# Kernel optimization log

Hardware: AMD Instinct MI355X
Metric: run time of the kernel (lower is better)

Reference implementation:

```python
import jax, jax.numpy as jnp
import numpy as np

N_WAY, K_SHOT = 5, 1
N_CLASSES = 64
D = 8


def _conv(x, w, b):
    y = jax.lax.conv_general_dilated(x, w, (2, 2), 'SAME',
                                     dimension_numbers=('NCHW', 'OIHW', 'NCHW'))
    return jax.nn.relu(y + b[None, :, None, None])


def setup_inputs() -> dict:
    key = jax.random.key(0)
    ks = jax.random.split(key, 12)
    b, s_sup, q, h, w = 4, N_WAY * K_SHOT, 1, 64, 64
    rnd = lambda k, shape: jax.random.normal(k, shape, jnp.float32) * 0.05
    return {
        'support_x': jax.random.normal(ks[0], (b, s_sup, 3, h, w), jnp.float32),
        'support_y': jax.random.randint(ks[1], (b, s_sup), 0, N_CLASSES),
        'query_x': jax.random.normal(ks[2], (b, q, 3, h, w), jnp.float32),
        'query_y': jax.random.randint(ks[3], (b, q), 0, N_CLASSES),
        'k1': rnd(ks[4], (32, 3, 3, 3)), 'bc1': jnp.zeros((32,), jnp.float32),
        'k2': rnd(ks[5], (48, 32, 3, 3)), 'bc2': jnp.zeros((48,), jnp.float32),
        'k3': rnd(ks[6], (64, 48, 3, 3)), 'bc3': jnp.zeros((64,), jnp.float32),
        'Wlog': rnd(ks[7], (64, N_CLASSES)), 'blog': jnp.zeros((N_CLASSES,), jnp.float32),
        'Wg1': rnd(ks[8], (132, 128)), 'bg1': jnp.zeros((128,), jnp.float32),
        'Wg2': rnd(ks[9], (128, 64)), 'bg2': jnp.zeros((64,), jnp.float32),
        'Wf1': rnd(ks[10], (64, 16)), 'bf1': jnp.zeros((16,), jnp.float32),
        'Wf2': rnd(ks[11], (16, 1)), 'bf2': jnp.zeros((1,), jnp.float32),
    }


def reference(support_x, support_y, query_x, query_y,
              k1, bc1, k2, bc2, k3, bc3, Wlog, blog,
              Wg1, bg1, Wg2, bg2, Wf1, bf1, Wf2, bf2):
    x = jnp.concatenate([support_x, query_x], axis=1)       # [b, s, 3, h, w]
    label = jnp.concatenate([support_y, query_y], axis=1)   # [b, s]
    b, s = label.shape
    h, w = x.shape[-2:]

    feat = x.reshape(b * s, 3, h, w)
    feat = _conv(feat, k1, bc1)
    feat = _conv(feat, k2, bc2)
    feat = _conv(feat, k3, bc3)                              # [b*s, c, D, D]
    c = feat.shape[1]
    logits = feat.mean(axis=(2, 3)) @ Wlog + blog            # [b*s, n_classes]

    # --- append normalized (i/d, j/d) coord channels ---
    ii = jnp.arange(D, dtype=feat.dtype) / D
    coord = jnp.stack([jnp.broadcast_to(ii[:, None], (D, D)),
                       jnp.broadcast_to(ii[None, :], (D, D))])        # [2, D, D]
    feat = feat.reshape(b, s, c, D, D)
    feat = jnp.concatenate([feat, jnp.broadcast_to(coord, (b, s, 2, D, D))], axis=2)
    c2 = c + 2
    m = D * D
    a = feat.reshape(b, s, c2, m).transpose(0, 1, 3, 2)      # [b, s, m, c2]

    # --- relation network g over all (set-pair, position-pair) combos ---
    # original: g(concat(x_i, x_j)) where x_i = x[b, j, :, q], x_j = x[b, i, :, p]
    # split first linear: concat @ Wg1 = x_i @ Wg1[:c2] + x_j @ Wg1[c2:]
    W1a, W1b = Wg1[:c2], Wg1[c2:]
    u = a @ W1a                                              # [b, s_j, m_q, 128]
    v = a @ W1b + bg1                                        # [b, s_i, m_p, 128]
    # hdd[b,i,j,q,p] = relu(u[b,j,q] + v[b,i,p])  -> [b, s, s, m, m, 128]
    hdd = jax.nn.relu(u[:, None, :, :, None, :] + v[:, :, None, None, :, :])
    g = jax.nn.relu(hdd @ Wg2 + bg2)                         # [b, s, s, m, m, 64]
    x_f = g.sum(axis=(3, 4))                                 # [b, s, s, 64]
    score = jax.nn.sigmoid(jax.nn.relu(x_f @ Wf1 + bf1) @ Wf2 + bf2)  # [b, s, s, 1]

    # --- losses ---
    logp = jax.nn.log_softmax(logits, axis=-1)
    lab = label.reshape(-1)
    cls_loss = -jnp.take_along_axis(logp, lab[:, None], axis=1).mean()

    y = (label[:, :, None] == label[:, None, :])[..., None].astype(score.dtype)
    P = score[..., 0]                                        # [b, s, s]
    Pt = P.transpose(0, 2, 1)
    sym, anti = 0.5 * (P + Pt), 0.5 * (P - Pt)
    sym_n = jnp.sqrt((sym ** 2).sum(axis=(1, 2)))            # Frobenius per batch
    anti_n = jnp.sqrt((anti ** 2).sum(axis=(1, 2)))
    sym_loss = ((sym_n - anti_n) / (sym_n + anti_n)).mean()
    euc_loss = ((score - y) ** 2).mean()
    rn_loss = euc_loss - 0.1 * sym_loss
    return (cls_loss, rn_loss, sym_loss)
```

## Files before the change

### kernel.cpp

```cpp
#include <hip/hip_runtime.h>

typedef _Float16 f16x8 __attribute__((ext_vector_type(8)));
typedef float f32x4 __attribute__((ext_vector_type(4)));
typedef unsigned u32x4 __attribute__((ext_vector_type(4)));

#define NB 192

__device__ __forceinline__ float ldw(const float* p) {
    return __uint_as_float(__hip_atomic_load((unsigned*)p, __ATOMIC_RELAXED,
                                             __HIP_MEMORY_SCOPE_SYSTEM));
}
__device__ __forceinline__ void stw(float* p, float x) {
    __hip_atomic_store((unsigned*)p, __float_as_uint(x), __ATOMIC_RELAXED,
                       __HIP_MEMORY_SCOPE_SYSTEM);
}
__device__ __forceinline__ unsigned ldu(const unsigned* p) {
    return __hip_atomic_load((unsigned*)p, __ATOMIC_RELAXED, __HIP_MEMORY_SCOPE_SYSTEM);
}
__device__ __forceinline__ void stu(unsigned* p, unsigned x) {
    __hip_atomic_store(p, x, __ATOMIC_RELAXED, __HIP_MEMORY_SCOPE_SYSTEM);
}

__device__ __forceinline__ void postf(int* fl, int bid) {
    asm volatile("s_waitcnt vmcnt(0) lgkmcnt(0)" ::: "memory");
    __hip_atomic_store(fl + bid, 1, __ATOMIC_RELAXED, __HIP_MEMORY_SCOPE_SYSTEM);
}
__device__ __forceinline__ void gbar(int* fl, int bid, int tid) {
    __syncthreads();
    if (tid == 0) postf(fl, bid);
    if (tid < 64) {
        int* p0 = fl + tid;
        for (;;) {
            int ok = (__hip_atomic_load(p0, __ATOMIC_RELAXED, __HIP_MEMORY_SCOPE_SYSTEM) == 1)
                   & (__hip_atomic_load(p0+64, __ATOMIC_RELAXED, __HIP_MEMORY_SCOPE_SYSTEM) == 1)
                   & (__hip_atomic_load(p0+128, __ATOMIC_RELAXED, __HIP_MEMORY_SCOPE_SYSTEM) == 1);
            if (__all(ok)) break;
            __builtin_amdgcn_s_sleep(2);
        }
    }
    __syncthreads();
    asm volatile("" ::: "memory");
}

__global__ void __launch_bounds__(512) mega3_k(
    const float* __restrict__ sx, const int* __restrict__ sy,
    const float* __restrict__ qx, const int* __restrict__ qy,
    const float* __restrict__ k1, const float* __restrict__ bc1,
    const float* __restrict__ k2, const float* __restrict__ bc2,
    const float* __restrict__ k3, const float* __restrict__ bc3,
    const float* __restrict__ Wlog, const float* __restrict__ blog,
    const float* __restrict__ Wg1, const float* __restrict__ bg1,
    const float* __restrict__ Wg2, const float* __restrict__ bg2,
    const float* __restrict__ Wf1, const float* __restrict__ bf1,
    const float* __restrict__ Wf2, const float* __restrict__ bf2,
    float* __restrict__ ws, float* __restrict__ out)
{
    __shared__ __align__(16) float smem[32768];
    const int tid = threadIdx.x;
    const int bid = blockIdx.x;

    float* feat1 = ws;
    float* feat2 = feat1 + 786432;
    float* feat3 = feat2 + 294912;
    float* mf    = feat3 + 98304;
    float* rv    = mf + 1536;
    float* Pmg   = rv + 64;
    unsigned* U32 = (unsigned*)(Pmg + 160);
    unsigned* V32 = U32 + 98304;
    int* flag0 = (int*)(V32 + 98304);
    int* flag1 = flag0 + 192;
    int* flag2 = flag1 + 192;
    int* flag3 = flag2 + 192;
    int* flagB = flag3 + 192;

    {
        int n = bid >> 3, ocq = bid & 7;
        int bi = n / 6, si = n % 6;
        const float* inp = (si < 5) ? sx + (size_t)((bi*5+si)*3)*4096
                                    : qx + (size_t)(bi*3)*4096;
        #pragma unroll
        for (int half = 0; half < 2; half++) {
            int px = tid + half*512;
            int oy = px >> 5, ox = px & 31;
            float tap[27];
            #pragma unroll
            for (int ic = 0; ic < 3; ic++)
                #pragma unroll
                for (int dy = 0; dy < 3; dy++)
                    #pragma unroll
                    for (int dx = 0; dx < 3; dx++) {
                        int iy = 2*oy+dy, ix = 2*ox+dx;
                        tap[ic*9+dy*3+dx] = (iy < 64 && ix < 64) ? inp[ic*4096 + iy*64 + ix] : 0.f;
                    }
            #pragma unroll
            for (int l = 0; l < 4; l++) {
                int oc = ocq*4 + l;
                float acc = bc1[oc];
                #pragma unroll
                for (int t = 0; t < 27; t++) acc += tap[t]*k1[oc*27 + t];
                stw(&feat1[(size_t)(n*32+oc)*1024 + px], fmaxf(acc, 0.f));
            }
        }
    }
    gbar(flag0, bid, tid);

    if (bid < 144) {
        int img = bid / 6, ocg = bid % 6;
        for (int k = 0; k < 64; k++) {
            int e = tid + 512*k;
            smem[e] = ldw(&feat1[(size_t)img*32768 + e]);
        }
        __syncthreads();
        int osub = tid >> 8, px = tid & 255;
        int oy = px >> 4, ox = px & 15;
        int ocb = ocg*8 + osub*4;
        float a0 = bc2[ocb], a1 = bc2[ocb+1], a2 = bc2[ocb+2], a3 = bc2[ocb+3];
        for (int ic = 0; ic < 32; ic++) {
            float tap[9];
            #pragma unroll
            for (int dy = 0; dy < 3; dy++)
                #pragma unroll
                for (int dx = 0; dx < 3; dx++) {
                    int iy = 2*oy+dy, ix = 2*ox+dx;
                    tap[dy*3+dx] = (iy < 32 && ix < 32) ? smem[ic*1024 + iy*32 + ix] : 0.f;
                }
            const float* wb = k2 + (size_t)ocb*288 + ic*9;
            #pragma unroll
            for (int t = 0; t < 9; t++) {
                a0 += tap[t]*wb[t];
                a1 += tap[t]*wb[288+t];
                a2 += tap[t]*wb[576+t];
                a3 += tap[t]*wb[864+t];
            }
        }
        size_t ob = (size_t)(img*48 + ocb)*256 + px;
        stw(&feat2[ob      ], fmaxf(a0, 0.f));
        stw(&feat2[ob + 256], fmaxf(a1, 0.f));
        stw(&feat2[ob + 512], fmaxf(a2, 0.f));
        stw(&feat2[ob + 768], fmaxf(a3, 0.f));
    }
    gbar(flag1, bid, tid);

    {
        int img = bid >> 3, ocg = bid & 7;
        __syncthreads();
        for (int k = 0; k < 24; k++) {
            int e = tid + 512*k;
            smem[e] = ldw(&feat2[(size_t)img*12288 + e]);
        }
        __syncthreads();
        int osub = tid >> 6, px = tid & 63;
        int oy = px >> 3, ox = px & 7;
        int oc = ocg*8 + osub;
        float a0 = bc3[oc];
        for (int ic = 0; ic < 48; ic++) {
            const float* wb = k3 + (size_t)oc*432 + ic*9;
            #pragma unroll
            for (int dy = 0; dy < 3; dy++)
                #pragma unroll
                for (int dx = 0; dx < 3; dx++) {
                    int iy = 2*oy+dy, ix = 2*ox+dx;
                    float tv = (iy < 16 && ix < 16) ? smem[ic*256 + iy*16 + ix] : 0.f;
                    a0 += tv * wb[dy*3+dx];
                }
        }
        float r0 = fmaxf(a0, 0.f);
        stw(&feat3[(size_t)(img*64 + oc)*64 + px], r0);
        #pragma unroll
        for (int off = 32; off >= 1; off >>= 1) r0 += __shfl_xor(r0, off, 64);
        if (px == 0) stw(&mf[img*64 + oc], r0 * (1.f/64.f));
    }
    gbar(flag2, bid, tid);

    if (bid < 48) {
        int bs = bid >> 1, ph = bid & 1;
        for (int k = 0; k < 8; k++) {
            int e = tid + 512*k;
            smem[e] = ldw(&feat3[(size_t)bs*4096 + e]);
        }
        __syncthreads();
        int cp = tid & 63;
        int sel = (tid >> 6) & 1;
        int pq = tid >> 7;
        int pbase = ph*32 + pq*8;
        float acc0[8], acc1[8];
        float b0 = sel ? bg1[2*cp] : 0.f;
        float b1 = sel ? bg1[2*cp+1] : 0.f;
        #pragma unroll
        for (int k = 0; k < 8; k++) { acc0[k] = b0; acc1[k] = b1; }
        const float* Wc = Wg1 + sel*66*128 + 2*cp;
        for (int c = 0; c < 64; c++) {
            float w0 = Wc[c*128], w1 = Wc[c*128 + 1];
            #pragma unroll
            for (int k = 0; k < 8; k++) {
                float a = smem[c*64 + pbase + k];
                acc0[k] += a*w0; acc1[k] += a*w1;
            }
        }
        #pragma unroll
        for (int c = 64; c < 66; c++) {
            float w0 = Wc[c*128], w1 = Wc[c*128 + 1];
            #pragma unroll
            for (int k = 0; k < 8; k++) {
                int p = pbase + k;
                float a = (c == 64) ? (float)(p>>3)*0.125f : (float)(p&7)*0.125f;
                acc0[k] += a*w0; acc1[k] += a*w1;
            }
        }
        unsigned* dst = sel ? V32 : U32;
        #pragma unroll
        for (int k = 0; k < 8; k++) {
            int p = pbase + k;
            unsigned lo = (unsigned)__builtin_bit_cast(unsigned short, (_Float16)acc0[k]);
            unsigned hi = (unsigned)__builtin_bit_cast(unsigned short, (_Float16)acc1[k]);
            stu(&dst[(size_t)bs*4096 + p*64 + cp], lo | (hi << 16));
        }
    } else if (bid < 72 && tid < 64) {
        int n = bid - 48;
        float s = blog[tid];
        for (int c = 0; c < 64; c++) s += ldw(&mf[n*64 + c]) * Wlog[c*64 + tid];
        float mx = s;
        #pragma unroll
        for (int off = 32; off >= 1; off >>= 1) mx = fmaxf(mx, __shfl_xor(mx, off, 64));
        float p = __expf(s - mx);
        float se = p;
        #pragma unroll
        for (int off = 32; off >= 1; off >>= 1) se += __shfl_xor(se, off, 64);
        int bi = n/6, si = n%6;
        int lab = (si < 5) ? sy[bi*5+si] : qy[bi];
        float s_lab = __shfl(s, lab, 64);
        if (tid == 0) stw(&rv[n], -(s_lab - mx - __logf(se)));
    }
    if (bid >= 144) {
        __syncthreads();
        if (tid == 0) postf(flag3, bid);
        return;
    }
    gbar(flag3, bid, tid);

    {
        int cb = bid;
        int b = cb / 36, rem = cb % 36;
        int j = rem / 6, i = rem % 6;
        int lane = tid & 63, wv8 = tid >> 6;
        int col = lane & 15, quad = lane >> 4;
        int qhalf = wv8 >> 2, pw = wv8 & 3;

        _Float16* Vsh = (_Float16*)smem;
        unsigned* Vsh32 = (unsigned*)smem;
        float* xfred = smem + 4096;
        float* xfl   = smem + 4608;
        float* hidl  = smem + 4672;

        int uimg = b*6 + i, vimg = b*6 + j;
        __syncthreads();
        #pragma unroll
        for (int k = 0; k < 8; k++) {
            int e = tid + 512*k;
            Vsh32[e] = ldu(&V32[(size_t)vimg*4096 + e]);
        }
        f16x8 uf[4];
        {
            const unsigned* up = U32 + (size_t)uimg*4096 + (pw*16 + col)*64 + quad*4;
            #pragma unroll
            for (int kt = 0; kt < 4; kt++) {
                u32x4 t;
                #pragma unroll
                for (int r = 0; r < 4; r++) t[r] = ldu(&up[kt*16 + r]);
                uf[kt] = __builtin_bit_cast(f16x8, t);
            }
        }
        f16x8 bf[4][4];
        #pragma unroll
        for (int kt = 0; kt < 4; kt++)
            #pragma unroll
            for (int nt = 0; nt < 4; nt++) {
                f16x8 t;
                #pragma unroll
                for (int jj = 0; jj < 8; jj++)
                    t[jj] = (_Float16)Wg2[(kt*32 + quad*8 + jj)*64 + nt*16 + col];
                bf[kt][nt] = t;
            }
        float bgv[4];
        #pragma unroll
        for (int nt = 0; nt < 4; nt++) bgv[nt] = bg2[nt*16 + col];
        __syncthreads();

        float sums[4] = {0.f,0.f,0.f,0.f};
        for (int qq = 0; qq < 32; qq++) {
            int q = qhalf*32 + qq;
            const _Float16* vp = &Vsh[q*128 + quad*8];
            f32x4 acc[4];
            #pragma unroll
            for (int nt = 0; nt < 4; nt++)
                acc[nt] = (f32x4){bgv[nt], bgv[nt], bgv[nt], bgv[nt]};
            #pragma unroll
            for (int kt = 0; kt < 4; kt++) {
                f16x8 vf = *(const f16x8*)&vp[kt*32];
                f16x8 af = uf[kt] + vf;
                af = __builtin_elementwise_max(af, (f16x8){0,0,0,0,0,0,0,0});
                #pragma unroll
                for (int nt = 0; nt < 4; nt++)
                    acc[nt] = __builtin_amdgcn_mfma_f32_16x16x32_f16(af, bf[kt][nt], acc[nt], 0, 0, 0);
            }
            #pragma unroll
            for (int nt = 0; nt < 4; nt++)
                #pragma unroll
                for (int rr = 0; rr < 4; rr++)
                    sums[nt] += fmaxf(acc[nt][rr], 0.f);
        }
        #pragma unroll
        for (int nt = 0; nt < 4; nt++) {
            sums[nt] += __shfl_xor(sums[nt], 16, 64);
            sums[nt] += __shfl_xor(sums[nt], 32, 64);
        }
        if (lane < 16) {
            #pragma unroll
            for (int nt = 0; nt < 4; nt++) xfred[wv8*64 + nt*16 + lane] = sums[nt];
        }
        __syncthreads();
        if (tid < 64) {
            float x = 0.f;
            #pragma unroll
            for (int w8 = 0; w8 < 8; w8++) x += xfred[w8*64 + tid];
            xfl[tid] = x;
        }
        __syncthreads();
        if (tid < 16) {
            float s = bf1[tid];
            for (int c = 0; c < 64; c++) s += xfl[c]*Wf1[c*16 + tid];
            hidl[tid] = fmaxf(s, 0.f);
        }
        __syncthreads();
        if (tid == 0) {
            float sc = bf2[0];
            #pragma unroll
            for (int h = 0; h < 16; h++) sc += hidl[h]*Wf2[h];
            stw(&Pmg[cb], 1.f/(1.f + __expf(-sc)));
            postf(flagB, cb);
        }
    }

    if (bid == 0) {
        if (tid < 64) {
            int* p0 = flagB + tid;
            for (;;) {
                int ok = (__hip_atomic_load(p0, __ATOMIC_RELAXED, __HIP_MEMORY_SCOPE_SYSTEM) == 1)
                       & (__hip_atomic_load(p0+64, __ATOMIC_RELAXED, __HIP_MEMORY_SCOPE_SYSTEM) == 1)
                       & ((tid < 16) ? (__hip_atomic_load(p0+128, __ATOMIC_RELAXED, __HIP_MEMORY_SCOPE_SYSTEM) == 1) : 1);
                if (__all(ok)) break;
                __builtin_amdgcn_s_sleep(2);
            }
        }
        __syncthreads();
        asm volatile("" ::: "memory");

        float* Pmsh = smem;
        int*   lab  = (int*)(smem + 160);
        float* red  = smem + 192;
        float* ratio= smem + 768;
        if (tid < 144) Pmsh[tid] = ldw(&Pmg[tid]);
        if (tid < 24) { int bi = tid/6, si = tid%6; lab[tid] = (si < 5) ? sy[bi*5+si] : qy[bi]; }
        __syncthreads();
        float e = 0.f;
        if (tid < 144) {
            int b = tid/36, r = tid%36, jj = r/6, ii = r%6;
            float y = (lab[b*6+jj] == lab[b*6+ii]) ? 1.f : 0.f;
            float d = Pmsh[tid] - y;
            e = d*d;
        }
        red[tid] = e;
        __syncthreads();
        for (int s = 256; s > 0; s >>= 1) {
            if (tid < s) red[tid] += red[tid+s];
            __syncthreads();
        }
        if (tid < 4) {
            float s2 = 0.f, a2 = 0.f;
            for (int jj = 0; jj < 6; jj++)
                for (int ii = 0; ii < 6; ii++) {
                    float pa = Pmsh[tid*36 + jj*6 + ii], pb = Pmsh[tid*36 + ii*6 + jj];
                    float sm = 0.5f*(pa+pb), an = 0.5f*(pa-pb);
                    s2 += sm*sm; a2 += an*an;
                }
            float sn = sqrtf(s2), anq = sqrtf(a2);
            ratio[tid] = (sn - anq)/(sn + anq);
        }
        __syncthreads();
        if (tid == 0) {
            float sl = 0.25f*(ratio[0]+ratio[1]+ratio[2]+ratio[3]);
            float euc = red[0] * (1.f/144.f);
            float cs = 0.f;
            for (int k = 0; k < 24; k++) cs += ldw(&rv[k]);
            out[0] = cs * (1.f/24.f);
            out[1] = euc - 0.1f*sl;
            out[2] = sl;
        }
    }
}

extern "C" void kernel_launch(void* const* d_in, const int* in_sizes, int n_in,
                              void* d_out, int out_size, void* d_ws, size_t ws_size,
                              hipStream_t stream) {
    (void)in_sizes; (void)n_in; (void)out_size; (void)ws_size;
    const float* sx   = (const float*)d_in[0];
    const int*   sy   = (const int*)  d_in[1];
    const float* qx   = (const float*)d_in[2];
    const int*   qy   = (const int*)  d_in[3];
    const float* k1   = (const float*)d_in[4];
    const float* bc1  = (const float*)d_in[5];
    const float* k2   = (const float*)d_in[6];
    const float* bc2  = (const float*)d_in[7];
    const float* k3   = (const float*)d_in[8];
    const float* bc3  = (const float*)d_in[9];
    const float* Wlog = (const float*)d_in[10];
    const float* blog = (const float*)d_in[11];
    const float* Wg1  = (const float*)d_in[12];
    const float* bg1  = (const float*)d_in[13];
    const float* Wg2  = (const float*)d_in[14];
    const float* bg2  = (const float*)d_in[15];
    const float* Wf1  = (const float*)d_in[16];
    const float* bf1  = (const float*)d_in[17];
    const float* Wf2  = (const float*)d_in[18];
    const float* bf2  = (const float*)d_in[19];
    float* ws  = (float*)d_ws;
    float* out = (float*)d_out;

    mega3_k<<<NB, 512, 0, stream>>>(sx, sy, qx, qy, k1, bc1, k2, bc2,
                                    k3, bc3, Wlog, blog, Wg1, bg1, Wg2, bg2,
                                    Wf1, bf1, Wf2, bf2, ws, out);
}
```

Baseline: 196.6 us.

## Restructure conv2/conv3 stages with row-register reuse, swizzled LDS, and 64-bit loads

Conv2 and conv3 are remapped so that each thread computes a whole output row for one output channel over a slice of input channels. Each thread loads input rows from LDS as float4 vectors into registers and reuses them across the 3 horizontal taps. Partial sums from the channel slices are then reduced through LDS. The LDS tile uses an XOR swizzle to reduce bank conflicts on the vector reads. All cross-block workspace loads switch from 32-bit to 64-bit relaxed atomic loads, which halves the number of load instructions. The cost is more registers, extra LDS reduction passes and syncs, and more complex indexing.

Measured after the change: 425.0 us. 116% more time.

```diff
diff --git a/kernel.cpp b/kernel.cpp
--- a/kernel.cpp
+++ b/kernel.cpp
@@ -2,7 +2,7 @@
 
 typedef _Float16 f16x8 __attribute__((ext_vector_type(8)));
 typedef float f32x4 __attribute__((ext_vector_type(4)));
-typedef unsigned u32x4 __attribute__((ext_vector_type(4)));
+typedef unsigned long long u64;
 
 #define NB 192
 
@@ -14,13 +14,9 @@
     __hip_atomic_store((unsigned*)p, __float_as_uint(x), __ATOMIC_RELAXED,
                        __HIP_MEMORY_SCOPE_SYSTEM);
 }
-__device__ __forceinline__ unsigned ldu(const unsigned* p) {
-    return __hip_atomic_load((unsigned*)p, __ATOMIC_RELAXED, __HIP_MEMORY_SCOPE_SYSTEM);
-}
-__device__ __forceinline__ void stu(unsigned* p, unsigned x) {
-    __hip_atomic_store(p, x, __ATOMIC_RELAXED, __HIP_MEMORY_SCOPE_SYSTEM);
-}
-
+__device__ __forceinline__ u64 ld64(const u64* p) {
+    return __hip_atomic_load(p, __ATOMIC_RELAXED, __HIP_MEMORY_SCOPE_SYSTEM);
+}
 __device__ __forceinline__ void postf(int* fl, int bid) {
     asm volatile("s_waitcnt vmcnt(0) lgkmcnt(0)" ::: "memory");
     __hip_atomic_store(fl + bid, 1, __ATOMIC_RELAXED, __HIP_MEMORY_SCOPE_SYSTEM);
@@ -42,7 +38,7 @@
     asm volatile("" ::: "memory");
 }
 
-__global__ void __launch_bounds__(512) mega3_k(
+__global__ void __launch_bounds__(512) mega4_k(
     const float* __restrict__ sx, const int* __restrict__ sy,
     const float* __restrict__ qx, const int* __restrict__ qy,
     const float* __restrict__ k1, const float* __restrict__ bc1,
@@ -106,77 +102,146 @@
 
     if (bid < 144) {
         int img = bid / 6, ocg = bid % 6;
-        for (int k = 0; k < 64; k++) {
-            int e = tid + 512*k;
-            smem[e] = ldw(&feat1[(size_t)img*32768 + e]);
-        }
-        __syncthreads();
-        int osub = tid >> 8, px = tid & 255;
-        int oy = px >> 4, ox = px & 15;
-        int ocb = ocg*8 + osub*4;
-        float a0 = bc2[ocb], a1 = bc2[ocb+1], a2 = bc2[ocb+2], a3 = bc2[ocb+3];
-        for (int ic = 0; ic < 32; ic++) {
-            float tap[9];
-            #pragma unroll
-            for (int dy = 0; dy < 3; dy++)
-                #pragma unroll
-                for (int dx = 0; dx < 3; dx++) {
-                    int iy = 2*oy+dy, ix = 2*ox+dx;
-                    tap[dy*3+dx] = (iy < 32 && ix < 32) ? smem[ic*1024 + iy*32 + ix] : 0.f;
+        const u64* src = (const u64*)(feat1 + (size_t)img*32768);
+        for (int b = 0; b < 4; b++) {
+            u64 t[8];
+            #pragma unroll
+            for (int j = 0; j < 8; j++) t[j] = ld64(&src[b*4096 + j*512 + tid]);
+            #pragma unroll
+            for (int j = 0; j < 8; j++) {
+                int d = (b*4096 + j*512 + tid)*2;
+                int ic = d >> 10, r = d & 1023, iy = r >> 5, ix = r & 31;
+                int la = (ic<<10) + (iy<<5) + (((((ix>>2)) ^ ((iy>>1)&7))<<2) | (ix&3));
+                ((u64*)smem)[la>>1] = t[j];
+            }
+        }
+        __syncthreads();
+        int oy = tid & 15, ocl = (tid>>4) & 7, ich = tid >> 7;
+        int oc = ocg*8 + ocl;
+        float acc[16];
+        #pragma unroll
+        for (int x = 0; x < 16; x++) acc[x] = 0.f;
+        for (int ic = ich*8; ic < ich*8+8; ic++) {
+            #pragma unroll
+            for (int dy = 0; dy < 3; dy++) {
+                int iy = 2*oy + dy;
+                float row[33];
+                if (iy < 32) {
+                    int sw = (iy>>1) & 7;
+                    #pragma unroll
+                    for (int q = 0; q < 8; q++) {
+                        f32x4 v = *(const f32x4*)&smem[(ic<<10) + (iy<<5) + ((q^sw)<<2)];
+                        row[q*4] = v[0]; row[q*4+1] = v[1]; row[q*4+2] = v[2]; row[q*4+3] = v[3];
+                    }
+                    row[32] = 0.f;
+                } else {
+                    #pragma unroll
+                    for (int x = 0; x < 33; x++) row[x] = 0.f;
                 }
-            const float* wb = k2 + (size_t)ocb*288 + ic*9;
-            #pragma unroll
-            for (int t = 0; t < 9; t++) {
-                a0 += tap[t]*wb[t];
-                a1 += tap[t]*wb[288+t];
-                a2 += tap[t]*wb[576+t];
-                a3 += tap[t]*wb[864+t];
-            }
-        }
-        size_t ob = (size_t)(img*48 + ocb)*256 + px;
-        stw(&feat2[ob      ], fmaxf(a0, 0.f));
-        stw(&feat2[ob + 256], fmaxf(a1, 0.f));
-        stw(&feat2[ob + 512], fmaxf(a2, 0.f));
-        stw(&feat2[ob + 768], fmaxf(a3, 0.f));
+                const float* wp = k2 + (size_t)oc*288 + ic*9 + dy*3;
+                float w0 = wp[0], w1 = wp[1], w2 = wp[2];
+                #pragma unroll
+                for (int ox = 0; ox < 16; ox++)
+                    acc[ox] += row[2*ox]*w0 + row[2*ox+1]*w1 + row[2*ox+2]*w2;
+            }
+        }
+        __syncthreads();
+        #pragma unroll
+        for (int q = 0; q < 4; q++)
+            *(f32x4*)&smem[ich*2048 + ocl*256 + oy*16 + q*4] =
+                (f32x4){acc[q*4], acc[q*4+1], acc[q*4+2], acc[q*4+3]};
+        __syncthreads();
+        #pragma unroll
+        for (int r = 0; r < 4; r++) {
+            int o = r*512 + tid;
+            float s = smem[o] + smem[2048+o] + smem[4096+o] + smem[6144+o];
+            int ocl2 = o >> 8, px = o & 255;
+            s += bc2[ocg*8 + ocl2];
+            stw(&feat2[(size_t)(img*48 + ocg*8 + ocl2)*256 + px], fmaxf(s, 0.f));
+        }
     }
     gbar(flag1, bid, tid);
 
     {
         int img = bid >> 3, ocg = bid & 7;
         __syncthreads();
-        for (int k = 0; k < 24; k++) {
-            int e = tid + 512*k;
-            smem[e] = ldw(&feat2[(size_t)img*12288 + e]);
-        }
-        __syncthreads();
-        int osub = tid >> 6, px = tid & 63;
-        int oy = px >> 3, ox = px & 7;
-        int oc = ocg*8 + osub;
-        float a0 = bc3[oc];
-        for (int ic = 0; ic < 48; ic++) {
-            const float* wb = k3 + (size_t)oc*432 + ic*9;
-            #pragma unroll
-            for (int dy = 0; dy < 3; dy++)
-                #pragma unroll
-                for (int dx = 0; dx < 3; dx++) {
-                    int iy = 2*oy+dy, ix = 2*ox+dx;
-                    float tv = (iy < 16 && ix < 16) ? smem[ic*256 + iy*16 + ix] : 0.f;
-                    a0 += tv * wb[dy*3+dx];
+        const u64* src = (const u64*)(feat2 + (size_t)img*12288);
+        for (int b = 0; b < 2; b++) {
+            u64 t[8];
+            #pragma unroll
+            for (int j = 0; j < 8; j++) {
+                int idx = b*4096 + j*512 + tid;
+                if (idx < 6144) t[j] = ld64(&src[idx]);
+            }
+            #pragma unroll
+            for (int j = 0; j < 8; j++) {
+                int idx = b*4096 + j*512 + tid;
+                if (idx < 6144) {
+                    int d = idx*2;
+                    int ic = d >> 8, r = d & 255, iy = r >> 4, ix = r & 15;
+                    int la = (ic<<8) + (iy<<4) + (((((ix>>2)) ^ ((iy>>1)&3))<<2) | (ix&3));
+                    ((u64*)smem)[la>>1] = t[j];
                 }
-        }
-        float r0 = fmaxf(a0, 0.f);
-        stw(&feat3[(size_t)(img*64 + oc)*64 + px], r0);
-        #pragma unroll
-        for (int off = 32; off >= 1; off >>= 1) r0 += __shfl_xor(r0, off, 64);
-        if (px == 0) stw(&mf[img*64 + oc], r0 * (1.f/64.f));
+            }
+        }
+        __syncthreads();
+        int oy = tid & 7, ocl = (tid>>3) & 7, ich = tid >> 6;
+        int oc = ocg*8 + ocl;
+        float acc[8];
+        #pragma unroll
+        for (int x = 0; x < 8; x++) acc[x] = 0.f;
+        for (int ic = ich*6; ic < ich*6+6; ic++) {
+            #pragma unroll
+            for (int dy = 0; dy < 3; dy++) {
+                int iy = 2*oy + dy;
+                float row[17];
+                if (iy < 16) {
+                    int sw = (iy>>1) & 3;
+                    #pragma unroll
+                    for (int q = 0; q < 4; q++) {
+                        f32x4 v = *(const f32x4*)&smem[(ic<<8) + (iy<<4) + ((q^sw)<<2)];
+                        row[q*4] = v[0]; row[q*4+1] = v[1]; row[q*4+2] = v[2]; row[q*4+3] = v[3];
+                    }
+                    row[16] = 0.f;
+                } else {
+                    #pragma unroll
+                    for (int x = 0; x < 17; x++) row[x] = 0.f;
+                }
+                const float* wp = k3 + (size_t)oc*432 + ic*9 + dy*3;
+                float w0 = wp[0], w1 = wp[1], w2 = wp[2];
+                #pragma unroll
+                for (int ox = 0; ox < 8; ox++)
+                    acc[ox] += row[2*ox]*w0 + row[2*ox+1]*w1 + row[2*ox+2]*w2;
+            }
+        }
+        __syncthreads();
+        *(f32x4*)&smem[ich*512 + ocl*64 + oy*8]     = (f32x4){acc[0],acc[1],acc[2],acc[3]};
+        *(f32x4*)&smem[ich*512 + ocl*64 + oy*8 + 4] = (f32x4){acc[4],acc[5],acc[6],acc[7]};
+        __syncthreads();
+        {
+            int ocl2 = tid >> 6, px = tid & 63;
+            float s = bc3[ocg*8 + ocl2];
+            #pragma unroll
+            for (int h = 0; h < 8; h++) s += smem[h*512 + tid];
+            float r0 = fmaxf(s, 0.f);
+            stw(&feat3[(size_t)(img*64 + ocg*8 + ocl2)*64 + px], r0);
+            #pragma unroll
+            for (int off = 32; off >= 1; off >>= 1) r0 += __shfl_xor(r0, off, 64);
+            if (px == 0) stw(&mf[img*64 + ocg*8 + ocl2], r0 * (1.f/64.f));
+        }
     }
     gbar(flag2, bid, tid);
 
     if (bid < 48) {
         int bs = bid >> 1, ph = bid & 1;
-        for (int k = 0; k < 8; k++) {
-            int e = tid + 512*k;
-            smem[e] = ldw(&feat3[(size_t)bs*4096 + e]);
+        __syncthreads();
+        const u64* src = (const u64*)(feat3 + (size_t)bs*4096);
+        {
+            u64 t[4];
+            #pragma unroll
+            for (int j = 0; j < 4; j++) t[j] = ld64(&src[j*512 + tid]);
+            #pragma unroll
+            for (int j = 0; j < 4; j++) ((u64*)smem)[j*512 + tid] = t[j];
         }
         __syncthreads();
         int cp = tid & 63;
@@ -213,7 +278,8 @@
             int p = pbase + k;
             unsigned lo = (unsigned)__builtin_bit_cast(unsigned short, (_Float16)acc0[k]);
             unsigned hi = (unsigned)__builtin_bit_cast(unsigned short, (_Float16)acc1[k]);
-            stu(&dst[(size_t)bs*4096 + p*64 + cp], lo | (hi << 16));
+            __hip_atomic_store(&dst[(size_t)bs*4096 + p*64 + cp], lo | (hi << 16),
+                               __ATOMIC_RELAXED, __HIP_MEMORY_SCOPE_SYSTEM);
         }
     } else if (bid < 72 && tid < 64) {
         int n = bid - 48;
@@ -247,27 +313,33 @@
         int qhalf = wv8 >> 2, pw = wv8 & 3;
 
         _Float16* Vsh = (_Float16*)smem;
-        unsigned* Vsh32 = (unsigned*)smem;
         float* xfred = smem + 4096;
         float* xfl   = smem + 4608;
         float* hidl  = smem + 4672;
 
         int uimg = b*6 + i, vimg = b*6 + j;
         __syncthreads();
-        #pragma unroll
-        for (int k = 0; k < 8; k++) {
-            int e = tid + 512*k;
-            Vsh32[e] = ldu(&V32[(size_t)vimg*4096 + e]);
+        {
+            const u64* src = (const u64*)(V32 + (size_t)vimg*4096);
+            u64 t[4];
+            #pragma unroll
+            for (int k = 0; k < 4; k++) t[k] = ld64(&src[k*512 + tid]);
+            #pragma unroll
+            for (int k = 0; k < 4; k++) ((u64*)smem)[k*512 + tid] = t[k];
         }
         f16x8 uf[4];
         {
-            const unsigned* up = U32 + (size_t)uimg*4096 + (pw*16 + col)*64 + quad*4;
+            const u64* up = (const u64*)(U32 + (size_t)uimg*4096 + (pw*16 + col)*64 + quad*4);
+            u64 t[8];
             #pragma unroll
             for (int kt = 0; kt < 4; kt++) {
-                u32x4 t;
-                #pragma unroll
-                for (int r = 0; r < 4; r++) t[r] = ldu(&up[kt*16 + r]);
-                uf[kt] = __builtin_bit_cast(f16x8, t);
+                t[kt*2]   = ld64(&up[kt*8]);
+                t[kt*2+1] = ld64(&up[kt*8 + 1]);
+            }
+            #pragma unroll
+            for (int kt = 0; kt < 4; kt++) {
+                u64 pair[2] = {t[kt*2], t[kt*2+1]};
+                uf[kt] = __builtin_bit_cast(f16x8, pair);
             }
         }
         f16x8 bf[4][4];
@@ -426,7 +498,7 @@
     float* ws  = (float*)d_ws;
     float* out = (float*)d_out;
 
-    mega3_k<<<NB, 512, 0, stream>>>(sx, sy, qx, qy, k1, bc1, k2, bc2,
+    mega4_k<<<NB, 512, 0, stream>>>(sx, sy, qx, qy, k1, bc1, k2, bc2,
                                     k3, bc3, Wlog, blog, Wg1, bg1, Wg2, bg2,
                                     Wf1, bf1, Wf2, bf2, ws, out);
 }
```

## Fuse per-image backbone and projection into one block with per-image dataflow flags

Applied to the files above, without the earlier changes.

Each of 24 images now runs conv1, conv2, conv3, the Wg1 projection and the classification logits entirely in one block's shared memory, instead of spreading each stage over 192 blocks joined by grid-wide barriers and global feature buffers. Pair blocks then wait only on flags for the two images they need rather than on a full grid barrier, and the grid shrinks to 144 blocks. This removes global round trips for intermediate features and most barrier latency, at the cost of much less parallelism in the backbone (24 blocks doing all the conv work) and a serial chain per image.

Result: slower. 288.0 us (+46.5%).

```diff
diff --git a/kernel.cpp b/kernel.cpp
--- a/kernel.cpp
+++ b/kernel.cpp
@@ -4,8 +4,6 @@
 typedef float f32x4 __attribute__((ext_vector_type(4)));
 typedef unsigned u32x4 __attribute__((ext_vector_type(4)));
 
-#define NB 192
-
 __device__ __forceinline__ float ldw(const float* p) {
     return __uint_as_float(__hip_atomic_load((unsigned*)p, __ATOMIC_RELAXED,
                                              __HIP_MEMORY_SCOPE_SYSTEM));
@@ -20,29 +18,15 @@
 __device__ __forceinline__ void stu(unsigned* p, unsigned x) {
     __hip_atomic_store(p, x, __ATOMIC_RELAXED, __HIP_MEMORY_SCOPE_SYSTEM);
 }
-
-__device__ __forceinline__ void postf(int* fl, int bid) {
+__device__ __forceinline__ void postf(int* fl, int idx) {
     asm volatile("s_waitcnt vmcnt(0) lgkmcnt(0)" ::: "memory");
-    __hip_atomic_store(fl + bid, 1, __ATOMIC_RELAXED, __HIP_MEMORY_SCOPE_SYSTEM);
-}
-__device__ __forceinline__ void gbar(int* fl, int bid, int tid) {
-    __syncthreads();
-    if (tid == 0) postf(fl, bid);
-    if (tid < 64) {
-        int* p0 = fl + tid;
-        for (;;) {
-            int ok = (__hip_atomic_load(p0, __ATOMIC_RELAXED, __HIP_MEMORY_SCOPE_SYSTEM) == 1)
-                   & (__hip_atomic_load(p0+64, __ATOMIC_RELAXED, __HIP_MEMORY_SCOPE_SYSTEM) == 1)
-                   & (__hip_atomic_load(p0+128, __ATOMIC_RELAXED, __HIP_MEMORY_SCOPE_SYSTEM) == 1);
-            if (__all(ok)) break;
-            __builtin_amdgcn_s_sleep(2);
-        }
-    }
-    __syncthreads();
-    asm volatile("" ::: "memory");
-}
-
-__global__ void __launch_bounds__(512) mega3_k(
+    __hip_atomic_store(fl + idx, 1, __ATOMIC_RELAXED, __HIP_MEMORY_SCOPE_SYSTEM);
+}
+__device__ __forceinline__ int ldflag(const int* fl, int idx) {
+    return __hip_atomic_load(fl + idx, __ATOMIC_RELAXED, __HIP_MEMORY_SCOPE_SYSTEM);
+}
+
+__global__ void __launch_bounds__(512) mega5_k(
     const float* __restrict__ sx, const int* __restrict__ sy,
     const float* __restrict__ qx, const int* __restrict__ qy,
     const float* __restrict__ k1, const float* __restrict__ bc1,
@@ -59,23 +43,16 @@
     const int tid = threadIdx.x;
     const int bid = blockIdx.x;
 
-    float* feat1 = ws;
-    float* feat2 = feat1 + 786432;
-    float* feat3 = feat2 + 294912;
-    float* mf    = feat3 + 98304;
-    float* rv    = mf + 1536;
+    float* rv    = ws;
     float* Pmg   = rv + 64;
     unsigned* U32 = (unsigned*)(Pmg + 160);
-    unsigned* V32 = U32 + 98304;
-    int* flag0 = (int*)(V32 + 98304);
-    int* flag1 = flag0 + 192;
-    int* flag2 = flag1 + 192;
-    int* flag3 = flag2 + 192;
-    int* flagB = flag3 + 192;
-
-    {
-        int n = bid >> 3, ocq = bid & 7;
-        int bi = n / 6, si = n % 6;
+    unsigned* V32 = U32 + 24*4096;
+    int* flagC   = (int*)(V32 + 24*4096);
+    int* flagB   = flagC + 64;
+
+    if (bid < 24) {
+        const int n = bid;
+        const int bi = n / 6, si = n % 6;
         const float* inp = (si < 5) ? sx + (size_t)((bi*5+si)*3)*4096
                                     : qx + (size_t)(bi*3)*4096;
         #pragma unroll
@@ -92,156 +69,146 @@
                         int iy = 2*oy+dy, ix = 2*ox+dx;
                         tap[ic*9+dy*3+dx] = (iy < 64 && ix < 64) ? inp[ic*4096 + iy*64 + ix] : 0.f;
                     }
-            #pragma unroll
-            for (int l = 0; l < 4; l++) {
-                int oc = ocq*4 + l;
-                float acc = bc1[oc];
-                #pragma unroll
-                for (int t = 0; t < 27; t++) acc += tap[t]*k1[oc*27 + t];
-                stw(&feat1[(size_t)(n*32+oc)*1024 + px], fmaxf(acc, 0.f));
-            }
-        }
+            for (int oc = 0; oc < 32; oc++) {
+                float a = bc1[oc];
+                #pragma unroll
+                for (int t = 0; t < 27; t++) a += tap[t]*k1[oc*27 + t];
+                smem[oc*1024 + px] = fmaxf(a, 0.f);
+            }
+        }
+        __syncthreads();
+
+        {
+            int px = tid & 255, grp = tid >> 8;
+            int oy = px >> 4, ox = px & 15;
+            float acc[24];
+            #pragma unroll
+            for (int o = 0; o < 24; o++) acc[o] = bc2[grp*24 + o];
+            for (int ic = 0; ic < 32; ic++) {
+                float tap[9];
+                #pragma unroll
+                for (int dy = 0; dy < 3; dy++)
+                    #pragma unroll
+                    for (int dx = 0; dx < 3; dx++) {
+                        int iy = 2*oy+dy, ix = 2*ox+dx;
+                        tap[dy*3+dx] = (iy < 32 && ix < 32) ? smem[ic*1024 + iy*32 + ix] : 0.f;
+                    }
+                #pragma unroll
+                for (int o = 0; o < 24; o++) {
+                    const float* wp = k2 + (size_t)(grp*24 + o)*288 + ic*9;
+                    #pragma unroll
+                    for (int t = 0; t < 9; t++) acc[o] += tap[t]*wp[t];
+                }
+            }
+            __syncthreads();
+            #pragma unroll
+            for (int o = 0; o < 24; o++)
+                smem[(grp*24 + o)*256 + px] = fmaxf(acc[o], 0.f);
+        }
+        __syncthreads();
+
+        {
+            int px3 = tid & 63, grp3 = tid >> 6;
+            int oy = px3 >> 3, ox = px3 & 7;
+            float a3[8];
+            #pragma unroll
+            for (int o = 0; o < 8; o++) a3[o] = bc3[grp3*8 + o];
+            for (int ic = 0; ic < 48; ic++) {
+                float tap[9];
+                #pragma unroll
+                for (int dy = 0; dy < 3; dy++)
+                    #pragma unroll
+                    for (int dx = 0; dx < 3; dx++) {
+                        int iy = 2*oy+dy, ix = 2*ox+dx;
+                        tap[dy*3+dx] = (iy < 16 && ix < 16) ? smem[ic*256 + iy*16 + ix] : 0.f;
+                    }
+                #pragma unroll
+                for (int o = 0; o < 8; o++) {
+                    const float* wp = k3 + (size_t)(grp3*8 + o)*432 + ic*9;
+                    #pragma unroll
+                    for (int t = 0; t < 9; t++) a3[o] += tap[t]*wp[t];
+                }
+            }
+            #pragma unroll
+            for (int o = 0; o < 8; o++) {
+                float r = fmaxf(a3[o], 0.f);
+                smem[16384 + (grp3*8 + o)*64 + px3] = r;
+                #pragma unroll
+                for (int off = 32; off >= 1; off >>= 1) r += __shfl_xor(r, off, 64);
+                if (px3 == 0) smem[20480 + grp3*8 + o] = r * (1.f/64.f);
+            }
+        }
+        __syncthreads();
+
+        {
+            int cp  = tid & 63;
+            int sel = (tid >> 6) & 1;
+            int pq  = tid >> 7;
+            int pbase = pq*16;
+            float a0[16], a1[16];
+            float b0 = sel ? bg1[2*cp] : 0.f;
+            float b1 = sel ? bg1[2*cp+1] : 0.f;
+            #pragma unroll
+            for (int k = 0; k < 16; k++) { a0[k] = b0; a1[k] = b1; }
+            const float* Wc = Wg1 + sel*66*128 + 2*cp;
+            for (int c = 0; c < 64; c++) {
+                float w0 = Wc[c*128], w1 = Wc[c*128 + 1];
+                #pragma unroll
+                for (int k = 0; k < 16; k++) {
+                    float a = smem[16384 + c*64 + pbase + k];
+                    a0[k] += a*w0; a1[k] += a*w1;
+                }
+            }
+            #pragma unroll
+            for (int c = 64; c < 66; c++) {
+                float w0 = Wc[c*128], w1 = Wc[c*128 + 1];
+                #pragma unroll
+                for (int k = 0; k < 16; k++) {
+                    int p = pbase + k;
+                    float a = (c == 64) ? (float)(p>>3)*0.125f : (float)(p&7)*0.125f;
+                    a0[k] += a*w0; a1[k] += a*w1;
+                }
+            }
+            unsigned* dst = (sel ? V32 : U32) + (size_t)n*4096;
+            #pragma unroll
+            for (int k = 0; k < 16; k++) {
+                int p = pbase + k;
+                unsigned lo = (unsigned)__builtin_bit_cast(unsigned short, (_Float16)a0[k]);
+                unsigned hi = (unsigned)__builtin_bit_cast(unsigned short, (_Float16)a1[k]);
+                stu(&dst[p*64 + cp], lo | (hi << 16));
+            }
+        }
+        if (tid < 64) {
+            float s = blog[tid];
+            for (int c = 0; c < 64; c++) s += smem[20480 + c] * Wlog[c*64 + tid];
+            float mx = s;
+            #pragma unroll
+            for (int off = 32; off >= 1; off >>= 1) mx = fmaxf(mx, __shfl_xor(mx, off, 64));
+            float p = __expf(s - mx);
+            float se = p;
+            #pragma unroll
+            for (int off = 32; off >= 1; off >>= 1) se += __shfl_xor(se, off, 64);
+            int lab = (si < 5) ? sy[bi*5+si] : qy[bi];
+            float s_lab = __shfl(s, lab, 64);
+            if (tid == 0) stw(&rv[n], -(s_lab - mx - __logf(se)));
+        }
+        __syncthreads();
+        if (tid == 0) postf(flagC, n);
     }
-    gbar(flag0, bid, tid);
-
-    if (bid < 144) {
-        int img = bid / 6, ocg = bid % 6;
-        for (int k = 0; k < 64; k++) {
-            int e = tid + 512*k;
-            smem[e] = ldw(&feat1[(size_t)img*32768 + e]);
-        }
-        __syncthreads();
-        int osub = tid >> 8, px = tid & 255;
-        int oy = px >> 4, ox = px & 15;
-        int ocb = ocg*8 + osub*4;
-        float a0 = bc2[ocb], a1 = bc2[ocb+1], a2 = bc2[ocb+2], a3 = bc2[ocb+3];
-        for (int ic = 0; ic < 32; ic++) {
-            float tap[9];
-            #pragma unroll
-            for (int dy = 0; dy < 3; dy++)
-                #pragma unroll
-                for (int dx = 0; dx < 3; dx++) {
-                    int iy = 2*oy+dy, ix = 2*ox+dx;
-                    tap[dy*3+dx] = (iy < 32 && ix < 32) ? smem[ic*1024 + iy*32 + ix] : 0.f;
-                }
-            const float* wb = k2 + (size_t)ocb*288 + ic*9;
-            #pragma unroll
-            for (int t = 0; t < 9; t++) {
-                a0 += tap[t]*wb[t];
-                a1 += tap[t]*wb[288+t];
-                a2 += tap[t]*wb[576+t];
-                a3 += tap[t]*wb[864+t];
-            }
-        }
-        size_t ob = (size_t)(img*48 + ocb)*256 + px;
-        stw(&feat2[ob      ], fmaxf(a0, 0.f));
-        stw(&feat2[ob + 256], fmaxf(a1, 0.f));
-        stw(&feat2[ob + 512], fmaxf(a2, 0.f));
-        stw(&feat2[ob + 768], fmaxf(a3, 0.f));
-    }
-    gbar(flag1, bid, tid);
-
-    {
-        int img = bid >> 3, ocg = bid & 7;
-        __syncthreads();
-        for (int k = 0; k < 24; k++) {
-            int e = tid + 512*k;
-            smem[e] = ldw(&feat2[(size_t)img*12288 + e]);
-        }
-        __syncthreads();
-        int osub = tid >> 6, px = tid & 63;
-        int oy = px >> 3, ox = px & 7;
-        int oc = ocg*8 + osub;
-        float a0 = bc3[oc];
-        for (int ic = 0; ic < 48; ic++) {
-            const float* wb = k3 + (size_t)oc*432 + ic*9;
-            #pragma unroll
-            for (int dy = 0; dy < 3; dy++)
-                #pragma unroll
-                for (int dx = 0; dx < 3; dx++) {
-                    int iy = 2*oy+dy, ix = 2*ox+dx;
-                    float tv = (iy < 16 && ix < 16) ? smem[ic*256 + iy*16 + ix] : 0.f;
-                    a0 += tv * wb[dy*3+dx];
-                }
-        }
-        float r0 = fmaxf(a0, 0.f);
-        stw(&feat3[(size_t)(img*64 + oc)*64 + px], r0);
-        #pragma unroll
-        for (int off = 32; off >= 1; off >>= 1) r0 += __shfl_xor(r0, off, 64);
-        if (px == 0) stw(&mf[img*64 + oc], r0 * (1.f/64.f));
-    }
-    gbar(flag2, bid, tid);
-
-    if (bid < 48) {
-        int bs = bid >> 1, ph = bid & 1;
-        for (int k = 0; k < 8; k++) {
-            int e = tid + 512*k;
-            smem[e] = ldw(&feat3[(size_t)bs*4096 + e]);
-        }
-        __syncthreads();
-        int cp = tid & 63;
-        int sel = (tid >> 6) & 1;
-        int pq = tid >> 7;
-        int pbase = ph*32 + pq*8;
-        float acc0[8], acc1[8];
-        float b0 = sel ? bg1[2*cp] : 0.f;
-        float b1 = sel ? bg1[2*cp+1] : 0.f;
-        #pragma unroll
-        for (int k = 0; k < 8; k++) { acc0[k] = b0; acc1[k] = b1; }
-        const float* Wc = Wg1 + sel*66*128 + 2*cp;
-        for (int c = 0; c < 64; c++) {
-            float w0 = Wc[c*128], w1 = Wc[c*128 + 1];
-            #pragma unroll
-            for (int k = 0; k < 8; k++) {
-                float a = smem[c*64 + pbase + k];
-                acc0[k] += a*w0; acc1[k] += a*w1;
-            }
-        }
-        #pragma unroll
-        for (int c = 64; c < 66; c++) {
-            float w0 = Wc[c*128], w1 = Wc[c*128 + 1];
-            #pragma unroll
-            for (int k = 0; k < 8; k++) {
-                int p = pbase + k;
-                float a = (c == 64) ? (float)(p>>3)*0.125f : (float)(p&7)*0.125f;
-                acc0[k] += a*w0; acc1[k] += a*w1;
-            }
-        }
-        unsigned* dst = sel ? V32 : U32;
-        #pragma unroll
-        for (int k = 0; k < 8; k++) {
-            int p = pbase + k;
-            unsigned lo = (unsigned)__builtin_bit_cast(unsigned short, (_Float16)acc0[k]);
-            unsigned hi = (unsigned)__builtin_bit_cast(unsigned short, (_Float16)acc1[k]);
-            stu(&dst[(size_t)bs*4096 + p*64 + cp], lo | (hi << 16));
-        }
-    } else if (bid < 72 && tid < 64) {
-        int n = bid - 48;
-        float s = blog[tid];
-        for (int c = 0; c < 64; c++) s += ldw(&mf[n*64 + c]) * Wlog[c*64 + tid];
-        float mx = s;
-        #pragma unroll
-        for (int off = 32; off >= 1; off >>= 1) mx = fmaxf(mx, __shfl_xor(mx, off, 64));
-        float p = __expf(s - mx);
-        float se = p;
-        #pragma unroll
-        for (int off = 32; off >= 1; off >>= 1) se += __shfl_xor(se, off, 64);
-        int bi = n/6, si = n%6;
-        int lab = (si < 5) ? sy[bi*5+si] : qy[bi];
-        float s_lab = __shfl(s, lab, 64);
-        if (tid == 0) stw(&rv[n], -(s_lab - mx - __logf(se)));
-    }
-    if (bid >= 144) {
-        __syncthreads();
-        if (tid == 0) postf(flag3, bid);
-        return;
-    }
-    gbar(flag3, bid, tid);
 
     {
         int cb = bid;
         int b = cb / 36, rem = cb % 36;
         int j = rem / 6, i = rem % 6;
+        int uimg = b*6 + i, vimg = b*6 + j;
+
+        if (tid == 0) {
+            while (!(ldflag(flagC, uimg) == 1 && ldflag(flagC, vimg) == 1))
+                __builtin_amdgcn_s_sleep(2);
+        }
+        __syncthreads();
+        asm volatile("" ::: "memory");
+
         int lane = tid & 63, wv8 = tid >> 6;
         int col = lane & 15, quad = lane >> 4;
         int qhalf = wv8 >> 2, pw = wv8 & 3;
@@ -252,22 +219,26 @@
         float* xfl   = smem + 4608;
         float* hidl  = smem + 4672;
 
-        int uimg = b*6 + i, vimg = b*6 + j;
-        __syncthreads();
-        #pragma unroll
-        for (int k = 0; k < 8; k++) {
-            int e = tid + 512*k;
-            Vsh32[e] = ldu(&V32[(size_t)vimg*4096 + e]);
+        {
+            const unsigned* src = V32 + (size_t)vimg*4096;
+            unsigned t[8];
+            #pragma unroll
+            for (int k = 0; k < 8; k++) t[k] = ldu(&src[k*512 + tid]);
+            #pragma unroll
+            for (int k = 0; k < 8; k++) Vsh32[k*512 + tid] = t[k];
         }
         f16x8 uf[4];
         {
             const unsigned* up = U32 + (size_t)uimg*4096 + (pw*16 + col)*64 + quad*4;
+            unsigned t[16];
+            #pragma unroll
+            for (int kt = 0; kt < 4; kt++)
+                #pragma unroll
+                for (int r = 0; r < 4; r++) t[kt*4+r] = ldu(&up[kt*16 + r]);
             #pragma unroll
             for (int kt = 0; kt < 4; kt++) {
-                u32x4 t;
-                #pragma unroll
-                for (int r = 0; r < 4; r++) t[r] = ldu(&up[kt*16 + r]);
-                uf[kt] = __builtin_bit_cast(f16x8, t);
+                u32x4 q4 = {t[kt*4], t[kt*4+1], t[kt*4+2], t[kt*4+3]};
+                uf[kt] = __builtin_bit_cast(f16x8, q4);
             }
         }
         f16x8 bf[4][4];
@@ -343,11 +314,10 @@
 
     if (bid == 0) {
         if (tid < 64) {
-            int* p0 = flagB + tid;
+            const int* p0 = flagB + tid;
             for (;;) {
-                int ok = (__hip_atomic_load(p0, __ATOMIC_RELAXED, __HIP_MEMORY_SCOPE_SYSTEM) == 1)
-                       & (__hip_atomic_load(p0+64, __ATOMIC_RELAXED, __HIP_MEMORY_SCOPE_SYSTEM) == 1)
-                       & ((tid < 16) ? (__hip_atomic_load(p0+128, __ATOMIC_RELAXED, __HIP_MEMORY_SCOPE_SYSTEM) == 1) : 1);
+                int ok = (ldflag(p0, 0) == 1) & (ldflag(p0, 64) == 1)
+                       & ((tid < 16) ? (ldflag(p0, 128) == 1) : 1);
                 if (__all(ok)) break;
                 __builtin_amdgcn_s_sleep(2);
             }
@@ -426,7 +396,7 @@
     float* ws  = (float*)d_ws;
     float* out = (float*)d_out;
 
-    mega3_k<<<NB, 512, 0, stream>>>(sx, sy, qx, qy, k1, bc1, k2, bc2,
-                                    k3, bc3, Wlog, blog, Wg1, bg1, Wg2, bg2,
-                                    Wf1, bf1, Wf2, bf2, ws, out);
-}
+    mega5_k<<<144, 512, 0, stream>>>(sx, sy, qx, qy, k1, bc1, k2, bc2,
+                                     k3, bc3, Wlog, blog, Wg1, bg1, Wg2, bg2,
+                                     Wf1, bf1, Wf2, bf2, ws, out);
+}
```
